# Performance work log

Measured on AMD Instinct MI355X. Metric: run time of the kernel, lower is better.

The kernel has to match this reference:

```python
import jax, jax.numpy as jnp
import numpy as np

B, T, C, E = 4, 4096, 2048, 64

def setup_inputs() -> dict:
    key = jax.random.key(0)
    k1, k2 = jax.random.split(key)
    hidden_states = jax.random.normal(k1, (B, T, C), dtype=jnp.float32)
    sim_matrix = jax.random.normal(k2, (C, E), dtype=jnp.float32)
    gates = jnp.zeros((E,), dtype=jnp.float32)
    return {"hidden_states": hidden_states, "sim_matrix": sim_matrix, "gates": gates}

def reference(hidden_states, sim_matrix, gates):
    b, t, c = hidden_states.shape
    e = sim_matrix.shape[1]
    x = hidden_states.reshape(-1, c)                     # [N, C], N = B*T
    token_affinity = x @ sim_matrix                      # [N, E]
    logits = token_affinity - jax.nn.sigmoid(gates)      # [N, E]
    gated_logits = jax.nn.relu(logits)                   # [N, E]
    mask = (gated_logits > 0).astype(gated_logits.dtype) # STE forward
    inactive = jnp.sum(mask, axis=-1) == 0               # [N]
    fallback_count = jnp.sum(inactive).astype(jnp.float32)
    k_fallback = e // 2
    _, fb_idx = jax.lax.top_k(logits, k_fallback)        # [N, k]
    rows = jnp.arange(x.shape[0])[:, None]
    fb_mask = jnp.zeros_like(mask).at[rows, fb_idx].set(1.0)
    # inactive tokens have all-zero mask, so fallback simply replaces it
    activation_mask = jnp.where(inactive[:, None], fb_mask, mask)
    neg_max = jnp.finfo(gated_logits.dtype).min          # == -finfo.max
    masked = jnp.where(activation_mask > 0, gated_logits, neg_max)
    active_expert_probs = jax.nn.softmax(masked, axis=-1).reshape(b, t, e)
    return (active_expert_probs, fallback_count,
            logits.reshape(b, t, e), activation_mask.reshape(b, t, e))
```

## Files before the change

kernel.cpp:

```cpp
#include <hip/hip_runtime.h>
#include <hip/hip_bf16.h>

#define N_TOK   16384
#define C_DIM   2048
#define E_DIM   64
#define P_OFF   (N_TOK * E_DIM)
#define FB_OFF  P_OFF
#define LG_OFF  (P_OFF + 1)
#define AM_OFF  (2 * P_OFF + 1)

typedef __attribute__((ext_vector_type(8))) short bf16x8;
typedef __attribute__((ext_vector_type(4))) float f32x4;

static __device__ __forceinline__ unsigned short f2bf_rtn(float f) {
    unsigned u = __float_as_uint(f);
    unsigned r = u + 0x7FFFu + ((u >> 16) & 1u);
    return (unsigned short)(r >> 16);
}
static __device__ __forceinline__ short f2bf_hw(float f) {
    __hip_bfloat16 h = __float2bfloat16(f);
    return *reinterpret_cast<short*>(&h);
}

__global__ void gating_prepack(const float* __restrict__ sim,
                               unsigned short* __restrict__ Bpk,
                               float* __restrict__ out) {
    int tid = blockIdx.x * 256 + threadIdx.x;
    if (tid == 0) out[FB_OFF] = 0.0f;
    if (tid >= C_DIM * E_DIM) return;
    int k = tid >> 6;
    int e = tid & 63;
    float v = sim[tid];
    int it = k >> 5;
    int gr = (k >> 3) & 3;
    int i  = k & 7;
    int lane = gr * 16 + (e & 15);
    int nb   = e >> 4;
    Bpk[it * 2048 + nb * 512 + lane * 8 + i] = f2bf_rtn(v);
}

__global__ __launch_bounds__(512, 8)
void gating_main(const float* __restrict__ x,
                 const unsigned short* __restrict__ Bpk,
                 const float* __restrict__ gates,
                 float* __restrict__ out) {
    __shared__ float red[8][16][64];

    const int tid = threadIdx.x;
    const int l   = tid & 63;
    const int w   = tid >> 6;
    const int row0 = blockIdx.x * 16;
    const int g    = l >> 4;
    const int e0   = l & 15;
    const float* xr = x + (size_t)(row0 + e0) * C_DIM + w * 256 + g * 8;
    const unsigned short* bw = Bpk + (size_t)w * 8 * 2048 + l * 8;

    f32x4 acc[4];
#pragma unroll
    for (int nb = 0; nb < 4; ++nb) acc[nb] = (f32x4)0.0f;

    for (int s = 0; s < 8; ++s) {
        const float* ap = xr + s * 32;
        float4 a0 = *(const float4*)ap;
        float4 a1 = *(const float4*)(ap + 4);
        bf16x8 ah;
        ah[0] = f2bf_hw(a0.x); ah[1] = f2bf_hw(a0.y);
        ah[2] = f2bf_hw(a0.z); ah[3] = f2bf_hw(a0.w);
        ah[4] = f2bf_hw(a1.x); ah[5] = f2bf_hw(a1.y);
        ah[6] = f2bf_hw(a1.z); ah[7] = f2bf_hw(a1.w);

        const unsigned short* bs = bw + s * 2048;
#pragma unroll
        for (int nb = 0; nb < 4; ++nb) {
            bf16x8 bf = *(const bf16x8*)(bs + nb * 512);
            acc[nb] = __builtin_amdgcn_mfma_f32_16x16x32_bf16(ah, bf, acc[nb], 0, 0, 0);
        }
    }

#pragma unroll
    for (int nb = 0; nb < 4; ++nb)
#pragma unroll
        for (int r = 0; r < 4; ++r)
            red[w][nb * 4 + r][l] = acc[nb][r];
    __syncthreads();

    if (w >= 4) return;

    float tot[4];
#pragma unroll
    for (int nb = 0; nb < 4; ++nb) {
        float t0 = 0.0f;
#pragma unroll
        for (int s = 0; s < 8; ++s) t0 += red[s][nb * 4 + w][l];
        tot[nb] = t0;
    }

    float sig[4];
#pragma unroll
    for (int nb = 0; nb < 4; ++nb)
        sig[nb] = 1.0f / (1.0f + expf(-gates[nb * 16 + e0]));

    const int t = row0 + g * 4 + w;
    float lg[4];
    bool  act[4];
    int   lcnt = 0;
    float lmax = -3.4e38f;
#pragma unroll
    for (int nb = 0; nb < 4; ++nb) {
        lg[nb]  = tot[nb] - sig[nb];
        act[nb] = lg[nb] > 0.0f;
        if (act[nb]) { lcnt++; lmax = fmaxf(lmax, lg[nb]); }
    }
    int cnt = lcnt;
    float mx = lmax;
#pragma unroll
    for (int m = 1; m < 16; m <<= 1) {
        cnt += __shfl_xor(cnt, m, 16);
        mx   = fmaxf(mx, __shfl_xor(mx, m, 16));
    }

    float p[4], am[4];
    if (cnt > 0) {
        float ex[4], ls = 0.0f;
#pragma unroll
        for (int nb = 0; nb < 4; ++nb) {
            ex[nb] = act[nb] ? expf(lg[nb] - mx) : 0.0f;
            ls += ex[nb];
        }
        float Z = ls;
#pragma unroll
        for (int m = 1; m < 16; m <<= 1) Z += __shfl_xor(Z, m, 16);
        float rz = 1.0f / Z;
#pragma unroll
        for (int nb = 0; nb < 4; ++nb) {
            p[nb]  = ex[nb] * rz;
            am[nb] = act[nb] ? 1.0f : 0.0f;
        }
    } else {
        unsigned selm = 0;
        for (int it = 0; it < 32; ++it) {
            float bv = -3.4e38f;
            int   bi = 127;
#pragma unroll
            for (int nb = 0; nb < 4; ++nb) {
                if (!((selm >> nb) & 1)) {
                    float v = lg[nb];
                    int   e = nb * 16 + e0;
                    if (v > bv || (v == bv && e < bi)) { bv = v; bi = e; }
                }
            }
#pragma unroll
            for (int m = 1; m < 16; m <<= 1) {
                float ov = __shfl_xor(bv, m, 16);
                int   oi = __shfl_xor(bi, m, 16);
                if (ov > bv || (ov == bv && oi < bi)) { bv = ov; bi = oi; }
            }
            if ((bi & 15) == e0) selm |= 1u << (bi >> 4);
        }
#pragma unroll
        for (int nb = 0; nb < 4; ++nb) {
            bool s_ = (selm >> nb) & 1;
            p[nb]  = s_ ? (1.0f / 32.0f) : 0.0f;
            am[nb] = s_ ? 1.0f : 0.0f;
        }
        if (e0 == 0) atomicAdd(&out[FB_OFF], 1.0f);
    }

#pragma unroll
    for (int nb = 0; nb < 4; ++nb) {
        int idx = t * 64 + nb * 16 + e0;
        out[idx]          = p[nb];
        out[LG_OFF + idx] = lg[nb];
        out[AM_OFF + idx] = am[nb];
    }
}

extern "C" void kernel_launch(void* const* d_in, const int* in_sizes, int n_in,
                              void* d_out, int out_size, void* d_ws, size_t ws_size,
                              hipStream_t stream) {
    const float* x     = (const float*)d_in[0];
    const float* sim   = (const float*)d_in[1];
    const float* gates = (const float*)d_in[2];
    float* out = (float*)d_out;
    unsigned short* Bpk = (unsigned short*)d_ws;

    gating_prepack<<<512, 256, 0, stream>>>(sim, Bpk, out);
    gating_main<<<1024, 512, 0, stream>>>(x, Bpk, gates, out);
}
```

Before: 38.17 us.

## Process 64 tokens per block with 16 K-split waves and bf16 partial-sum reduction

Each block now handles 64 tokens with 1024 threads, and each of 16 waves covers a 128-wide K slice. Within a wave, the B fragments loaded for a K step are reused across four row groups. Partial sums are stored to LDS as bf16 to keep the enlarged reduction buffer small, and all 16 waves now take part in the epilogue. Rounding the partials to bf16 before summing adds numerical error to the logits, which can flip threshold decisions, and the larger block may reduce occupancy.

After: 40.53 us. 6.2% more time.

```diff
diff --git a/kernel.cpp b/kernel.cpp
--- a/kernel.cpp
+++ b/kernel.cpp
@@ -16,6 +16,9 @@
     unsigned u = __float_as_uint(f);
     unsigned r = u + 0x7FFFu + ((u >> 16) & 1u);
     return (unsigned short)(r >> 16);
+}
+static __device__ __forceinline__ float bf2f(unsigned short h) {
+    return __uint_as_float(((unsigned)h) << 16);
 }
 static __device__ __forceinline__ short f2bf_hw(float f) {
     __hip_bfloat16 h = __float2bfloat16(f);
@@ -39,59 +42,71 @@
     Bpk[it * 2048 + nb * 512 + lane * 8 + i] = f2bf_rtn(v);
 }
 
-__global__ __launch_bounds__(512, 8)
+__global__ __launch_bounds__(1024, 4)
 void gating_main(const float* __restrict__ x,
                  const unsigned short* __restrict__ Bpk,
                  const float* __restrict__ gates,
                  float* __restrict__ out) {
-    __shared__ float red[8][16][64];
+    __shared__ unsigned short red[16][64][66];
 
     const int tid = threadIdx.x;
     const int l   = tid & 63;
     const int w   = tid >> 6;
-    const int row0 = blockIdx.x * 16;
+    const int row0 = blockIdx.x * 64;
     const int g    = l >> 4;
     const int e0   = l & 15;
-    const float* xr = x + (size_t)(row0 + e0) * C_DIM + w * 256 + g * 8;
-    const unsigned short* bw = Bpk + (size_t)w * 8 * 2048 + l * 8;
-
-    f32x4 acc[4];
-#pragma unroll
-    for (int nb = 0; nb < 4; ++nb) acc[nb] = (f32x4)0.0f;
-
-    for (int s = 0; s < 8; ++s) {
-        const float* ap = xr + s * 32;
-        float4 a0 = *(const float4*)ap;
-        float4 a1 = *(const float4*)(ap + 4);
-        bf16x8 ah;
-        ah[0] = f2bf_hw(a0.x); ah[1] = f2bf_hw(a0.y);
-        ah[2] = f2bf_hw(a0.z); ah[3] = f2bf_hw(a0.w);
-        ah[4] = f2bf_hw(a1.x); ah[5] = f2bf_hw(a1.y);
-        ah[6] = f2bf_hw(a1.z); ah[7] = f2bf_hw(a1.w);
-
+
+    const float* xbase = x + (size_t)(row0 + e0) * C_DIM + w * 128 + g * 8;
+    const unsigned short* bw = Bpk + (size_t)w * 4 * 2048 + l * 8;
+
+    f32x4 acc[4][4];
+#pragma unroll
+    for (int rg = 0; rg < 4; ++rg)
+#pragma unroll
+        for (int nb = 0; nb < 4; ++nb) acc[rg][nb] = (f32x4)0.0f;
+
+    for (int s = 0; s < 4; ++s) {
         const unsigned short* bs = bw + s * 2048;
-#pragma unroll
-        for (int nb = 0; nb < 4; ++nb) {
-            bf16x8 bf = *(const bf16x8*)(bs + nb * 512);
-            acc[nb] = __builtin_amdgcn_mfma_f32_16x16x32_bf16(ah, bf, acc[nb], 0, 0, 0);
-        }
-    }
-
-#pragma unroll
-    for (int nb = 0; nb < 4; ++nb)
-#pragma unroll
-        for (int r = 0; r < 4; ++r)
-            red[w][nb * 4 + r][l] = acc[nb][r];
+        bf16x8 bf[4];
+#pragma unroll
+        for (int nb = 0; nb < 4; ++nb)
+            bf[nb] = *(const bf16x8*)(bs + nb * 512);
+
+#pragma unroll
+        for (int rg = 0; rg < 4; ++rg) {
+            const float* ap = xbase + (size_t)rg * 16 * C_DIM + s * 32;
+            float4 a0 = *(const float4*)ap;
+            float4 a1 = *(const float4*)(ap + 4);
+            bf16x8 ah;
+            ah[0] = f2bf_hw(a0.x); ah[1] = f2bf_hw(a0.y);
+            ah[2] = f2bf_hw(a0.z); ah[3] = f2bf_hw(a0.w);
+            ah[4] = f2bf_hw(a1.x); ah[5] = f2bf_hw(a1.y);
+            ah[6] = f2bf_hw(a1.z); ah[7] = f2bf_hw(a1.w);
+#pragma unroll
+            for (int nb = 0; nb < 4; ++nb)
+                acc[rg][nb] = __builtin_amdgcn_mfma_f32_16x16x32_bf16(ah, bf[nb], acc[rg][nb], 0, 0, 0);
+        }
+    }
+
+#pragma unroll
+    for (int rg = 0; rg < 4; ++rg)
+#pragma unroll
+        for (int nb = 0; nb < 4; ++nb)
+#pragma unroll
+            for (int r = 0; r < 4; ++r)
+                red[w][rg * 16 + g * 4 + r][nb * 16 + e0] = f2bf_rtn(acc[rg][nb][r]);
     __syncthreads();
 
-    if (w >= 4) return;
+    const int tloc = w * 4 + g;
+    const int t    = row0 + tloc;
 
     float tot[4];
 #pragma unroll
     for (int nb = 0; nb < 4; ++nb) {
         float t0 = 0.0f;
 #pragma unroll
-        for (int s = 0; s < 8; ++s) t0 += red[s][nb * 4 + w][l];
+        for (int s = 0; s < 16; ++s)
+            t0 += bf2f(red[s][tloc][nb * 16 + e0]);
         tot[nb] = t0;
     }
 
@@ -100,7 +115,6 @@
     for (int nb = 0; nb < 4; ++nb)
         sig[nb] = 1.0f / (1.0f + expf(-gates[nb * 16 + e0]));
 
-    const int t = row0 + g * 4 + w;
     float lg[4];
     bool  act[4];
     int   lcnt = 0;
@@ -185,5 +199,5 @@
     unsigned short* Bpk = (unsigned short*)d_ws;
 
     gating_prepack<<<512, 256, 0, stream>>>(sim, Bpk, out);
-    gating_main<<<1024, 512, 0, stream>>>(x, Bpk, gates, out);
-}
+    gating_main<<<256, 1024, 0, stream>>>(x, Bpk, gates, out);
+}
```
